# Performance work log

Measured on AMD Instinct MI355X. Metric: run time of the kernel, lower is better.

The kernel has to match this reference:

```python
import jax, jax.numpy as jnp
import numpy as np

MARGIN = 0.3
NORM = 2.0  # p-norm used by both pairwise() and PairwiseDistance

M, C = 65536, 256   # n*h*w pixels, feature channels
K, P, Q = 20, 2048, 2048  # classes 1..nclass-1, positives, negatives per class


def setup_inputs() -> dict:
    key = jax.random.key(0)
    k1, k2, k3 = jax.random.split(key, 3)
    features = jax.random.normal(k1, (M, C), dtype=jnp.float32)
    pos_idx = jax.random.randint(k2, (K, P), 0, M)
    neg_idx = jax.random.randint(k3, (K, Q), 0, M)
    return {"features": features, "pos_idx": pos_idx, "neg_idx": neg_idx}


def _pairwise(x, y):
    # torch: clamp(xx - 2xy + yy, 0); (dis + eps) ** (1/norm)
    eps = 0.0001 / x.shape[1]
    xx = jnp.sum(x * x, axis=1)           # [P]
    yy = jnp.sum(y * y, axis=1)           # [Q]
    xy = x @ y.T                           # [P,Q] GEMM
    dis = jnp.clip(xx[:, None] - 2.0 * xy + yy[None, :], 0.0)
    return (dis + eps) ** (1.0 / NORM)


def _pdist(x1, x2):
    # PairwiseDistance: (clamp(sum(|x1-x2|^p), 0) + eps) ** (1/p)
    eps = 0.0001 / x1.shape[1]
    out = jnp.sum(jnp.abs(x1 - x2) ** NORM, axis=1)
    return (jnp.clip(out, 0.0) + eps) ** (1.0 / NORM)


def _class_loss(pos, neg):
    # hard mining on detached features (indices only, as in generate_triplet_simple)
    pos_d = jax.lax.stop_gradient(pos)
    neg_d = jax.lax.stop_gradient(neg)
    hp = jnp.argmax(_pairwise(pos_d, pos_d), axis=1)   # hardest positive per anchor
    hn = jnp.argmin(_pairwise(pos_d, neg_d), axis=1)   # hardest negative per anchor
    d_p = _pdist(pos, pos[hp])
    d_n = _pdist(pos, neg[hn])
    return jnp.mean(jnp.clip(MARGIN + d_p - d_n, 0.0))


def reference(features, pos_idx, neg_idx):
    f = jax.nn.sigmoid(features)          # torch.sigmoid(features)
    pos = f[pos_idx]                      # [K,P,C]
    neg = f[neg_idx]                      # [K,Q,C]
    losses = jax.vmap(_class_loss)(pos, neg)  # per-class triplet losses
    return jnp.sum(losses)                # loss accumulated over classes
```

## Files before the change

### kernel.cpp

```cpp
#include <hip/hip_runtime.h>
#include <stdint.h>

#define M_ROWS 65536
#define C_DIM  256
#define K_CLS  20
#define P_POS  2048
#define MARGIN_F 0.3f
#define EPS_D (0.0001f / 256.0f)
#define SCALE1 0x7F7F7F7Fu

typedef float floatx4 __attribute__((ext_vector_type(4)));
typedef int   intx8   __attribute__((ext_vector_type(8)));
union Frag8 { intx8 v; uint4 q[2]; };

__device__ __forceinline__ void async_copy16(const void* g, void* l) {
    __builtin_amdgcn_global_load_lds(
        (const __attribute__((address_space(1))) void*)g,
        (__attribute__((address_space(3))) void*)l, 16, 0, 0);
}
__device__ __forceinline__ float sigm(float x) { return 1.f / (1.f + __expf(-x)); }

__global__ __launch_bounds__(256) void sigmoid_norm_k(
        const float* __restrict__ feat,
        unsigned int* __restrict__ S8,
        float* __restrict__ xx,
        unsigned int* __restrict__ hp,
        unsigned int* __restrict__ hn) {
    {
        const int idx = blockIdx.x * 256 + threadIdx.x;
        if (idx < K_CLS * P_POS) { hp[idx] = 0u; hn[idx] = 0xFFFFFFFFu; }
    }
    const int wave = threadIdx.x >> 6, lane = threadIdx.x & 63;
    const int row = blockIdx.x * 4 + wave;
    const float4 v = *(const float4*)(feat + (size_t)row * C_DIM + lane * 4);

    const int p01 = __builtin_amdgcn_cvt_pk_fp8_f32(sigm(v.x), sigm(v.y), 0, false);
    const int p23 = __builtin_amdgcn_cvt_pk_fp8_f32(sigm(v.z), sigm(v.w), 0, false);
    const unsigned int packed = (unsigned int)(p01 & 0xFFFF) | ((unsigned int)p23 << 16);
    S8[(size_t)row * 64 + lane] = packed;

    const float q0 = __builtin_amdgcn_cvt_f32_fp8(p01, 0);
    const float q1 = __builtin_amdgcn_cvt_f32_fp8(p01, 1);
    const float q2 = __builtin_amdgcn_cvt_f32_fp8(p23, 0);
    const float q3 = __builtin_amdgcn_cvt_f32_fp8(p23, 1);
    float sum = q0 * q0 + q1 * q1 + q2 * q2 + q3 * q3;
#pragma unroll
    for (int off = 32; off; off >>= 1) sum += __shfl_down(sum, off);
    if (lane == 0) xx[row] = sum;
}

__global__ __launch_bounds__(256, 3) void select_k(
        const unsigned int* __restrict__ S8,
        const float* __restrict__ xx,
        const int* __restrict__ pos_idx,
        const int* __restrict__ neg_idx,
        unsigned int* __restrict__ hp,
        unsigned int* __restrict__ hn) {
    __shared__ __align__(16) unsigned char Bt[2][32 * 256];
    __shared__ float yyL[512];

    const int tid    = threadIdx.x;
    const int w      = tid >> 6;
    const int lane   = tid & 63;
    const int lane15 = lane & 15;
    const int quad   = lane >> 4;

    const int bid    = blockIdx.x;
    const int ctid   = bid % 40;
    const int rest   = bid / 40;
    const int i_blk  = rest >> 2;
    const int jq     = rest & 3;
    const int k      = ctid >> 1;
    const int isNeg  = ctid & 1;
    const int i0     = i_blk * 256;
    const int j0     = jq * 512;

    const int* __restrict__ idxA = pos_idx + k * P_POS;
    const int* __restrict__ idxB = (isNeg ? neg_idx : pos_idx) + k * P_POS;
    unsigned int* outKey         = (isNeg ? hn : hp) + k * P_POS;

    const char* S8B = (const char*)S8;

    const int rl  = lane >> 4;
    const int cch = lane & 15;
    int rloc[2], soff[2];
#pragma unroll
    for (int c = 0; c < 2; ++c) {
        rloc[c] = (w * 2 + c) * 4 + rl;
        soff[c] = (cch ^ (rloc[c] & 15)) << 4;
    }

    int g_st[2];
#pragma unroll
    for (int c = 0; c < 2; ++c) g_st[c] = idxB[j0 + rloc[c]];
#pragma unroll
    for (int c = 0; c < 2; ++c)
        async_copy16(S8B + ((size_t)(uint32_t)g_st[c] << 8) + soff[c],
                     (char*)&Bt[0][0] + (w * 2 + c) * 1024);
#pragma unroll
    for (int c = 0; c < 2; ++c) g_st[c] = idxB[j0 + 32 + rloc[c]];

#pragma unroll
    for (int t = 0; t < 2; ++t) {
        const int jj = t * 256 + tid;
        yyL[jj] = xx[idxB[j0 + jj]];
    }

    Frag8 A_reg[4][2];
#pragma unroll
    for (int si = 0; si < 4; ++si) {
        const int gi = idxA[i0 + w * 64 + si * 16 + lane15];
        const char* rb = S8B + ((size_t)(uint32_t)gi << 8) + quad * 32;
#pragma unroll
        for (int s = 0; s < 2; ++s) {
            A_reg[si][s].q[0] = *(const uint4*)(rb + s * 128);
            A_reg[si][s].q[1] = *(const uint4*)(rb + s * 128 + 16);
        }
    }

    int blo[2], bhi[2];
#pragma unroll
    for (int s = 0; s < 2; ++s) {
        const int c0 = s * 8 + quad * 2;
        blo[s] = lane15 * 256 + ((c0 ^ lane15) << 4);
        bhi[s] = lane15 * 256 + (((c0 + 1) ^ lane15) << 4);
    }

    float bestv[16];
    const float binit = isNeg ? 3.4e38f : -3.4e38f;
#pragma unroll
    for (int t = 0; t < 16; ++t) bestv[t] = binit;

#pragma unroll 2
    for (int jc = 0; jc < 16; ++jc) {
        __syncthreads();

        const float yv0 = yyL[(jc << 5) + lane15];
        const float yv1 = yyL[(jc << 5) + 16 + lane15];

        if (jc < 15) {
            char* lb = (char*)(&Bt[(jc + 1) & 1][0]);
#pragma unroll
            for (int c = 0; c < 2; ++c)
                async_copy16(S8B + ((size_t)(uint32_t)g_st[c] << 8) + soff[c],
                             lb + (w * 2 + c) * 1024);
        }
        {
            const int nt = j0 + (jc < 14 ? jc + 2 : 15) * 32;
#pragma unroll
            for (int c = 0; c < 2; ++c) g_st[c] = idxB[nt + rloc[c]];
        }

        const char* Bb = (const char*)(&Bt[jc & 1][0]);
        floatx4 acc[2][4];
#pragma unroll
        for (int ct = 0; ct < 2; ++ct)
#pragma unroll
            for (int si = 0; si < 4; ++si)
                acc[ct][si] = (floatx4){0.f, 0.f, 0.f, 0.f};

#pragma unroll
        for (int s = 0; s < 2; ++s) {
            Frag8 bf0, bf1;
            bf0.q[0] = *(const uint4*)(Bb + blo[s]);
            bf0.q[1] = *(const uint4*)(Bb + bhi[s]);
            bf1.q[0] = *(const uint4*)(Bb + blo[s] + 4096);
            bf1.q[1] = *(const uint4*)(Bb + bhi[s] + 4096);
#pragma unroll
            for (int si = 0; si < 4; ++si)
                acc[0][si] = __builtin_amdgcn_mfma_scale_f32_16x16x128_f8f6f4(
                    A_reg[si][s].v, bf0.v, acc[0][si], 0, 0,
                    0, SCALE1, 0, SCALE1);
#pragma unroll
            for (int si = 0; si < 4; ++si)
                acc[1][si] = __builtin_amdgcn_mfma_scale_f32_16x16x128_f8f6f4(
                    A_reg[si][s].v, bf1.v, acc[1][si], 0, 0,
                    0, SCALE1, 0, SCALE1);
        }

        const uint32_t jb0 = (uint32_t)((j0 + (jc << 5)) | lane15);
        const uint32_t jb1 = jb0 | 16u;
#pragma unroll
        for (int ct = 0; ct < 2; ++ct) {
            const float yv = ct ? yv1 : yv0;
            const uint32_t jb = ct ? jb1 : jb0;
#pragma unroll
            for (int si = 0; si < 4; ++si)
#pragma unroll
                for (int r = 0; r < 4; ++r) {
                    const float g = fmaf(-2.f, acc[ct][si][r], yv);
                    const float enc = __uint_as_float(
                        (__float_as_uint(g) & 0xFFFFF800u) | jb);
                    const int slot = si * 4 + r;
                    bestv[slot] = isNeg ? fminf(bestv[slot], enc)
                                        : fmaxf(bestv[slot], enc);
                }
        }
    }

#pragma unroll
    for (int slot = 0; slot < 16; ++slot) {
#pragma unroll
        for (int off = 1; off < 16; off <<= 1) {
            const float ov = __shfl_xor(bestv[slot], off);
            bestv[slot] = isNeg ? fminf(bestv[slot], ov) : fmaxf(bestv[slot], ov);
        }
    }
    if (lane15 == 0) {
#pragma unroll
        for (int si = 0; si < 4; ++si)
#pragma unroll
            for (int r = 0; r < 4; ++r) {
                const int row = w * 64 + si * 16 + quad * 4 + r;
                const uint32_t u = __float_as_uint(bestv[si * 4 + r]);
                const uint32_t key = (u & 0x80000000u) ? ~u : (u | 0x80000000u);
                if (isNeg) atomicMin(&outKey[i0 + row], key);
                else       atomicMax(&outKey[i0 + row], key);
            }
    }
}

#define ACC16(UA, UP, UN)                                                     \
    {                                                                         \
        float xa, d;                                                          \
        xa = __builtin_amdgcn_cvt_f32_fp8((int)(UA), 0);                      \
        d = xa - __builtin_amdgcn_cvt_f32_fp8((int)(UP), 0); dp += d * d;     \
        d = xa - __builtin_amdgcn_cvt_f32_fp8((int)(UN), 0); dn += d * d;     \
        xa = __builtin_amdgcn_cvt_f32_fp8((int)(UA), 1);                      \
        d = xa - __builtin_amdgcn_cvt_f32_fp8((int)(UP), 1); dp += d * d;     \
        d = xa - __builtin_amdgcn_cvt_f32_fp8((int)(UN), 1); dn += d * d;     \
        xa = __builtin_amdgcn_cvt_f32_fp8((int)(UA), 2);                      \
        d = xa - __builtin_amdgcn_cvt_f32_fp8((int)(UP), 2); dp += d * d;     \
        d = xa - __builtin_amdgcn_cvt_f32_fp8((int)(UN), 2); dn += d * d;     \
        xa = __builtin_amdgcn_cvt_f32_fp8((int)(UA), 3);                      \
        d = xa - __builtin_amdgcn_cvt_f32_fp8((int)(UP), 3); dp += d * d;     \
        d = xa - __builtin_amdgcn_cvt_f32_fp8((int)(UN), 3); dn += d * d;     \
    }

__global__ __launch_bounds__(256) void loss_k(
        const unsigned int* __restrict__ S8,
        const int* __restrict__ pos_idx,
        const int* __restrict__ neg_idx,
        const unsigned int* __restrict__ hp,
        const unsigned int* __restrict__ hn,
        float* __restrict__ terms) {
    const int tid    = threadIdx.x;
    const int lane15 = tid & 15;
    const int grp    = tid >> 4;
    const int a      = blockIdx.x * 16 + grp;
    const int k      = a >> 11;
    const int i      = a & 2047;
    const int* pidx = pos_idx + (k << 11);
    const int* nidx = neg_idx + (k << 11);
    const unsigned int kp = hp[a], kn = hn[a];
    const int jp = (int)((kp & 0x80000000u) ? (kp & 2047u) : ((~kp) & 2047u));
    const int jn = (int)((kn & 0x80000000u) ? (kn & 2047u) : ((~kn) & 2047u));
    const int ga = pidx[i];
    const int gp = pidx[jp];
    const int gn = nidx[jn];

    const char* S8B = (const char*)S8;
    const uint4 va = *(const uint4*)(S8B + ((size_t)(uint32_t)ga << 8) + lane15 * 16);
    const uint4 vp = *(const uint4*)(S8B + ((size_t)(uint32_t)gp << 8) + lane15 * 16);
    const uint4 vn = *(const uint4*)(S8B + ((size_t)(uint32_t)gn << 8) + lane15 * 16);

    float dp = 0.f, dn = 0.f;
    ACC16(va.x, vp.x, vn.x)
    ACC16(va.y, vp.y, vn.y)
    ACC16(va.z, vp.z, vn.z)
    ACC16(va.w, vp.w, vn.w)

#pragma unroll
    for (int off = 1; off < 16; off <<= 1) {
        dp += __shfl_xor(dp, off);
        dn += __shfl_xor(dn, off);
    }
    if (lane15 == 0) {
        const float d_p = sqrtf(fmaxf(dp, 0.f) + EPS_D);
        const float d_n = sqrtf(fmaxf(dn, 0.f) + EPS_D);
        terms[a] = fmaxf(MARGIN_F + d_p - d_n, 0.f);
    }
}

__global__ __launch_bounds__(1024) void reduce_k(
        const float* __restrict__ terms, float* __restrict__ out) {
    __shared__ float red[1024];
    float s = 0.f;
    for (int i = threadIdx.x; i < K_CLS * P_POS; i += 1024) s += terms[i];
    red[threadIdx.x] = s;
    __syncthreads();
    for (int off = 512; off; off >>= 1) {
        if ((int)threadIdx.x < off) red[threadIdx.x] += red[threadIdx.x + off];
        __syncthreads();
    }
    if (threadIdx.x == 0) out[0] = red[0] * (1.0f / (float)P_POS);
}

extern "C" void kernel_launch(void* const* d_in, const int* in_sizes, int n_in,
                              void* d_out, int out_size, void* d_ws, size_t ws_size,
                              hipStream_t stream) {
    const float* feat    = (const float*)d_in[0];
    const int*   pos_idx = (const int*)d_in[1];
    const int*   neg_idx = (const int*)d_in[2];

    char* ws = (char*)d_ws;
    unsigned int* S8 = (unsigned int*)ws;
    float*        xx = (float*)(ws + 16777216);
    unsigned int* hp = (unsigned int*)(ws + 17039360);
    unsigned int* hn = (unsigned int*)(ws + 17203200);
    float*     terms = (float*)(ws + 17367040);

    sigmoid_norm_k<<<M_ROWS / 4, 256, 0, stream>>>(feat, S8, xx, hp, hn);

    select_k<<<32 * 40, 256, 0, stream>>>(S8, xx, pos_idx, neg_idx, hp, hn);

    loss_k<<<(K_CLS * P_POS) / 16, 256, 0, stream>>>(S8, pos_idx, neg_idx, hp, hn, terms);

    reduce_k<<<1, 1024, 0, stream>>>(terms, (float*)d_out);
}
```

Before: 173.2 us.

## Fold -2·xy+yy into MFMA via negated A and scale, deepen B pipeline

The A fragments are negated by flipping the fp8 sign bits, and the MFMA uses an A scale of 2 with yy preloaded as the accumulator, so each MFMA yields yy-2xy directly and the per-element fma is gone. The B-tile staging grows from a double buffer to a four-slot ring. Gather indices are cached in LDS up front, and two column tiles are processed per barrier with explicit vmcnt waits, halving barrier count. Occupancy hint rises to 4 blocks, at the cost of more LDS per block and hand-managed wait counts that must match the issued async copies.

```diff
diff --git a/kernel.cpp b/kernel.cpp
--- a/kernel.cpp
+++ b/kernel.cpp
@@ -8,6 +8,7 @@
 #define MARGIN_F 0.3f
 #define EPS_D (0.0001f / 256.0f)
 #define SCALE1 0x7F7F7F7Fu
+#define SCALE2 0x80808080u
 
 typedef float floatx4 __attribute__((ext_vector_type(4)));
 typedef int   intx8   __attribute__((ext_vector_type(8)));
@@ -19,6 +20,11 @@
         (__attribute__((address_space(3))) void*)l, 16, 0, 0);
 }
 __device__ __forceinline__ float sigm(float x) { return 1.f / (1.f + __expf(-x)); }
+
+__device__ __forceinline__ void negA(Frag8& f) {
+#pragma unroll
+    for (int t = 0; t < 8; ++t) f.v[t] ^= (int)0x80808080u;
+}
 
 __global__ __launch_bounds__(256) void sigmoid_norm_k(
         const float* __restrict__ feat,
@@ -49,15 +55,16 @@
     if (lane == 0) xx[row] = sum;
 }
 
-__global__ __launch_bounds__(256, 3) void select_k(
+__global__ __launch_bounds__(256, 4) void select_k(
         const unsigned int* __restrict__ S8,
         const float* __restrict__ xx,
         const int* __restrict__ pos_idx,
         const int* __restrict__ neg_idx,
         unsigned int* __restrict__ hp,
         unsigned int* __restrict__ hn) {
-    __shared__ __align__(16) unsigned char Bt[2][32 * 256];
+    __shared__ __align__(16) unsigned char Bt[4][32 * 256];
     __shared__ float yyL[512];
+    __shared__ int   idxL[512];
 
     const int tid    = threadIdx.x;
     const int w      = tid >> 6;
@@ -81,29 +88,17 @@
 
     const char* S8B = (const char*)S8;
 
-    const int rl  = lane >> 4;
-    const int cch = lane & 15;
-    int rloc[2], soff[2];
-#pragma unroll
-    for (int c = 0; c < 2; ++c) {
-        rloc[c] = (w * 2 + c) * 4 + rl;
-        soff[c] = (cch ^ (rloc[c] & 15)) << 4;
-    }
-
-    int g_st[2];
-#pragma unroll
-    for (int c = 0; c < 2; ++c) g_st[c] = idxB[j0 + rloc[c]];
-#pragma unroll
-    for (int c = 0; c < 2; ++c)
-        async_copy16(S8B + ((size_t)(uint32_t)g_st[c] << 8) + soff[c],
-                     (char*)&Bt[0][0] + (w * 2 + c) * 1024);
-#pragma unroll
-    for (int c = 0; c < 2; ++c) g_st[c] = idxB[j0 + 32 + rloc[c]];
+    const int rl    = lane >> 4;
+    const int cch   = lane & 15;
+    const int rloc0 = w * 8 + rl;
+    const int soff0 = (cch ^ (rloc0 & 15)) << 4;
 
 #pragma unroll
     for (int t = 0; t < 2; ++t) {
         const int jj = t * 256 + tid;
-        yyL[jj] = xx[idxB[j0 + jj]];
+        const int gj = idxB[j0 + jj];
+        idxL[jj] = gj;
+        yyL[jj]  = xx[gj];
     }
 
     Frag8 A_reg[4][2];
@@ -115,86 +110,88 @@
         for (int s = 0; s < 2; ++s) {
             A_reg[si][s].q[0] = *(const uint4*)(rb + s * 128);
             A_reg[si][s].q[1] = *(const uint4*)(rb + s * 128 + 16);
+            negA(A_reg[si][s]);
         }
     }
 
-    int blo[2], bhi[2];
-#pragma unroll
-    for (int s = 0; s < 2; ++s) {
-        const int c0 = s * 8 + quad * 2;
-        blo[s] = lane15 * 256 + ((c0 ^ lane15) << 4);
-        bhi[s] = lane15 * 256 + (((c0 + 1) ^ lane15) << 4);
-    }
+    const int blo0 = lane15 * 256 + (((quad * 2) ^ lane15) << 4);
 
     float bestv[16];
     const float binit = isNeg ? 3.4e38f : -3.4e38f;
 #pragma unroll
     for (int t = 0; t < 16; ++t) bestv[t] = binit;
 
-#pragma unroll 2
-    for (int jc = 0; jc < 16; ++jc) {
-        __syncthreads();
-
-        const float yv0 = yyL[(jc << 5) + lane15];
-        const float yv1 = yyL[(jc << 5) + 16 + lane15];
-
-        if (jc < 15) {
-            char* lb = (char*)(&Bt[(jc + 1) & 1][0]);
-#pragma unroll
-            for (int c = 0; c < 2; ++c)
-                async_copy16(S8B + ((size_t)(uint32_t)g_st[c] << 8) + soff[c],
-                             lb + (w * 2 + c) * 1024);
+    __syncthreads();
+
+#pragma unroll
+    for (int t = 0; t < 4; ++t) {
+        const int b  = (t << 5) + rloc0;
+        const int r0 = idxL[b];
+        const int r1 = idxL[b + 4];
+        char* lb = (char*)&Bt[t][0] + (w * 2) * 1024;
+        async_copy16(S8B + ((size_t)(uint32_t)r0 << 8) + soff0,        lb);
+        async_copy16(S8B + ((size_t)(uint32_t)r1 << 8) + (soff0 ^ 64), lb + 1024);
+    }
+
+#pragma unroll
+    for (int p = 0; p < 8; ++p) {
+        if (p == 0) { asm volatile("s_waitcnt vmcnt(4)" ::: "memory"); }
+        else        { asm volatile("s_waitcnt vmcnt(0)" ::: "memory"); }
+        __builtin_amdgcn_s_barrier();
+        __builtin_amdgcn_sched_barrier(0);
+
+        if (p >= 1 && p <= 6) {
+            const int t = 2 * p + 2;
+#pragma unroll
+            for (int u = 0; u < 2; ++u) {
+                const int b  = ((t + u) << 5) + rloc0;
+                const int r0 = idxL[b];
+                const int r1 = idxL[b + 4];
+                char* lb = (char*)&Bt[(t + u) & 3][0] + (w * 2) * 1024;
+                async_copy16(S8B + ((size_t)(uint32_t)r0 << 8) + soff0,        lb);
+                async_copy16(S8B + ((size_t)(uint32_t)r1 << 8) + (soff0 ^ 64), lb + 1024);
+            }
         }
-        {
-            const int nt = j0 + (jc < 14 ? jc + 2 : 15) * 32;
-#pragma unroll
-            for (int c = 0; c < 2; ++c) g_st[c] = idxB[nt + rloc[c]];
-        }
-
-        const char* Bb = (const char*)(&Bt[jc & 1][0]);
-        floatx4 acc[2][4];
-#pragma unroll
-        for (int ct = 0; ct < 2; ++ct)
-#pragma unroll
-            for (int si = 0; si < 4; ++si)
-                acc[ct][si] = (floatx4){0.f, 0.f, 0.f, 0.f};
-
-#pragma unroll
-        for (int s = 0; s < 2; ++s) {
-            Frag8 bf0, bf1;
-            bf0.q[0] = *(const uint4*)(Bb + blo[s]);
-            bf0.q[1] = *(const uint4*)(Bb + bhi[s]);
-            bf1.q[0] = *(const uint4*)(Bb + blo[s] + 4096);
-            bf1.q[1] = *(const uint4*)(Bb + bhi[s] + 4096);
-#pragma unroll
-            for (int si = 0; si < 4; ++si)
-                acc[0][si] = __builtin_amdgcn_mfma_scale_f32_16x16x128_f8f6f4(
-                    A_reg[si][s].v, bf0.v, acc[0][si], 0, 0,
-                    0, SCALE1, 0, SCALE1);
-#pragma unroll
-            for (int si = 0; si < 4; ++si)
-                acc[1][si] = __builtin_amdgcn_mfma_scale_f32_16x16x128_f8f6f4(
-                    A_reg[si][s].v, bf1.v, acc[1][si], 0, 0,
-                    0, SCALE1, 0, SCALE1);
-        }
-
-        const uint32_t jb0 = (uint32_t)((j0 + (jc << 5)) | lane15);
-        const uint32_t jb1 = jb0 | 16u;
-#pragma unroll
-        for (int ct = 0; ct < 2; ++ct) {
-            const float yv = ct ? yv1 : yv0;
-            const uint32_t jb = ct ? jb1 : jb0;
-#pragma unroll
-            for (int si = 0; si < 4; ++si)
-#pragma unroll
-                for (int r = 0; r < 4; ++r) {
-                    const float g = fmaf(-2.f, acc[ct][si][r], yv);
-                    const float enc = __uint_as_float(
-                        (__float_as_uint(g) & 0xFFFFF800u) | jb);
-                    const int slot = si * 4 + r;
-                    bestv[slot] = isNeg ? fminf(bestv[slot], enc)
-                                        : fmaxf(bestv[slot], enc);
-                }
+
+#pragma unroll
+        for (int u = 0; u < 2; ++u) {
+            const int jc = 2 * p + u;
+            const char* Bb = (const char*)&Bt[jc & 3][0];
+#pragma unroll
+            for (int ct = 0; ct < 2; ++ct) {
+                const float yv = yyL[(jc << 5) + (ct << 4) + lane15];
+                const floatx4 yv4 = {yv, yv, yv, yv};
+                const int cto = ct << 12;
+                Frag8 bf;
+                bf.q[0] = *(const uint4*)(Bb + (blo0      ) + cto);
+                bf.q[1] = *(const uint4*)(Bb + (blo0 ^ 16 ) + cto);
+                floatx4 acc[4];
+#pragma unroll
+                for (int si = 0; si < 4; ++si)
+                    acc[si] = __builtin_amdgcn_mfma_scale_f32_16x16x128_f8f6f4(
+                        A_reg[si][0].v, bf.v, yv4, 0, 0,
+                        0, SCALE2, 0, SCALE1);
+                bf.q[0] = *(const uint4*)(Bb + (blo0 ^ 128) + cto);
+                bf.q[1] = *(const uint4*)(Bb + (blo0 ^ 144) + cto);
+#pragma unroll
+                for (int si = 0; si < 4; ++si)
+                    acc[si] = __builtin_amdgcn_mfma_scale_f32_16x16x128_f8f6f4(
+                        A_reg[si][1].v, bf.v, acc[si], 0, 0,
+                        0, SCALE2, 0, SCALE1);
+
+                const uint32_t jb =
+                    (uint32_t)((j0 + (jc << 5) + (ct << 4)) | lane15);
+#pragma unroll
+                for (int si = 0; si < 4; ++si)
+#pragma unroll
+                    for (int r = 0; r < 4; ++r) {
+                        const float e = __uint_as_float(
+                            (__float_as_uint(acc[si][r]) & 0xFFFFF800u) | jb);
+                        const int slot = si * 4 + r;
+                        bestv[slot] = isNeg ? fminf(bestv[slot], e)
+                                            : fmaxf(bestv[slot], e);
+                    }
+            }
         }
     }
 
```

Result: slower. 244.1 us (+40.9%).
